# Kernel tuning notes

Hardware: AMD Instinct MI355X
Metric: run time of the kernel (lower is better)

The kernel has to match this reference:

```python
import jax, jax.numpy as jnp
import numpy as np

B, T, D, M, L = 4, 2048, 256, 128, 16
P = M * L  # max_pair_cnt


def setup_inputs() -> dict:
    key = jax.random.key(0)
    ks = jax.random.split(key, 11)
    head = jax.random.normal(ks[0], (B, P, T), jnp.float32) * 0.05
    tail = jax.random.normal(ks[1], (B, P, T), jnp.float32) * 0.05
    x = jax.random.normal(ks[2], (B, T, D), jnp.float32)
    coref_mention_position = jax.random.uniform(ks[3], (B, M, T), jnp.float32)
    lab = jax.random.uniform(ks[4], (B, P, 2), jnp.float32) + 1e-3
    coref_label = lab / lab.sum(-1, keepdims=True)  # already-softmaxed target
    coref_label_mask = jax.random.randint(ks[5], (B, P), 0, 2).astype(bool)
    lens = jnp.full((B, M), L, jnp.int32)  # uniform segment lengths
    w1 = jax.random.normal(ks[6], (3 * D, D), jnp.float32) / np.sqrt(3 * D).astype(np.float32)
    b1 = jnp.zeros((D,), jnp.float32)
    w2 = jax.random.normal(ks[7], (D, 2), jnp.float32) / np.sqrt(D).astype(np.float32)
    b2 = jnp.zeros((2,), jnp.float32)
    return {"head": head, "tail": tail, "lens": lens, "x": x,
            "coref_mention_position": coref_mention_position,
            "coref_label": coref_label, "coref_label_mask": coref_label_mask,
            "w1": w1, "b1": b1, "w2": w2, "b2": b2}


def reference(head, tail, lens, x, coref_mention_position, coref_label,
              coref_label_mask, w1, b1, w2, b2):
    # bmm-based gather of mention reps: [B,P,T] @ [B,T,D] -> [B,P,D]
    head_rep = jnp.einsum('bpt,btd->bpd', head, x)
    tail_rep = jnp.einsum('bpt,btd->bpd', tail, x)
    feat = jnp.concatenate([head_rep, tail_rep, head_rep * tail_rep], axis=-1)
    logits = jax.nn.relu(feat @ w1 + b1) @ w2 + b2  # [B,P,2]

    # ragged split_n_pad -> per-mention top-1 select (uniform lens == L -> reshape)
    scores = logits[..., 1].reshape(B, M, L)            # [B,M,L]
    max_idx = jnp.argmax(scores, axis=-1)               # [B,M]
    max_val = jnp.max(scores, axis=-1)                  # [B,M] (raw logit, as in source)
    tail_seg = tail_rep.reshape(B, M, L, D)
    sel = jnp.take_along_axis(tail_seg, max_idx[:, :, None, None], axis=2)[:, :, 0, :]
    coref_rep_m = sel * max_val[:, :, None]             # [B,M,D]

    # scatter-bmm merge back into sequence: [B,T,M] @ [B,M,D] -> [B,T,D]
    coref_rep = jnp.einsum('bmt,bmd->btd', coref_mention_position, coref_rep_m)
    output = x + coref_rep

    # KLDivLoss(reduction='mean') over masked pairs
    logq = jax.nn.log_softmax(logits, axis=-1)
    lab = coref_label
    pw = jnp.where(lab > 0, lab * jnp.log(jnp.maximum(lab, 1e-38)), 0.0) - lab * logq
    n = jnp.sum(coref_label_mask).astype(jnp.float32)
    loss = jnp.where(coref_label_mask[..., None], pw, 0.0).sum() / (n * 2.0)
    return output, loss
```

## Files before the change

kernel.cpp:

```cpp
#include <hip/hip_runtime.h>
#include <hip/hip_bf16.h>
#include <stdint.h>

#define TAU 0.35f

typedef __attribute__((ext_vector_type(8))) short bf16x8;
typedef __attribute__((ext_vector_type(4))) float f32x4;

__device__ __forceinline__ unsigned short f2bf(float f) {
  __bf16 h = (__bf16)f;
  return __builtin_bit_cast(unsigned short, h);
}
__device__ __forceinline__ float bf2f(unsigned short u) {
  unsigned int v = ((unsigned int)u) << 16;
  return __builtin_bit_cast(float, v);
}
__device__ __forceinline__ void async_copy16(const void* g, void* l) {
  __builtin_amdgcn_global_load_lds(
      (const __attribute__((address_space(1))) unsigned int*)g,
      (__attribute__((address_space(3))) unsigned int*)l, 16, 0, 0);
}

__global__ __launch_bounds__(256) void k_prep(
    const float* __restrict__ x, const float* __restrict__ w1,
    const float* __restrict__ b2,
    unsigned short* __restrict__ xt, unsigned short* __restrict__ w1t,
    float* __restrict__ logits, int* __restrict__ njobs) {
  __shared__ float tileS[64][65];
  int bx = blockIdx.x, tid = threadIdx.x;
  if (bx == 0 && tid == 0) *njobs = 0;
  if (bx < 64) {
    int i = bx * 256 + tid;
    logits[i] = b2[i & 1];
  }
  int j = tid & 63, i0 = tid >> 6;
  if (bx < 512) {
    int b = bx >> 7, t6 = (bx >> 2) & 31, d6 = bx & 3;
    const float* src = x + ((size_t)b * 2048 + (size_t)t6 * 64) * 256 + d6 * 64;
    for (int i = i0; i < 64; i += 4) tileS[i][j] = src[(size_t)i * 256 + j];
    __syncthreads();
    unsigned short* dst = xt + ((size_t)b * 256 + (size_t)d6 * 64) * 2048 + t6 * 64;
    for (int r = i0; r < 64; r += 4) dst[(size_t)r * 2048 + j] = f2bf(tileS[j][r]);
  } else {
    int wt = bx - 512;
    int k6 = wt >> 2, n6 = wt & 3;
    const float* src = w1 + ((size_t)k6 * 64) * 256 + n6 * 64;
    for (int i = i0; i < 64; i += 4) tileS[i][j] = src[(size_t)i * 256 + j];
    __syncthreads();
    unsigned short* dst = w1t + ((size_t)n6 * 64) * 768 + k6 * 64;
    for (int r = i0; r < 64; r += 4) dst[(size_t)r * 768 + j] = f2bf(tileS[j][r]);
  }
}

__global__ __launch_bounds__(256, 4) void k_gemm_rep(
    const float* __restrict__ head, const float* __restrict__ tail,
    const unsigned short* __restrict__ xt,
    float* __restrict__ hrep, float* __restrict__ trep) {
  __shared__ unsigned short As[2][4096];
  __shared__ unsigned short Bs[2][4096];
  int bx = blockIdx.x;
  int ntile = bx >> 8;
  int g = bx & 255;
  int b = g >> 6, mtile = g & 63;
  const float* Asrc = ((mtile < 32) ? head : tail) +
                      ((size_t)(b * 2048 + (mtile & 31) * 64)) * 2048;
  float* Crep = (mtile < 32) ? hrep : trep;
  const unsigned short* Bsrc = xt + ((size_t)(b * 256 + ntile * 64)) * 2048;

  int tid = threadIdx.x, lane = tid & 63, w = tid >> 6;

  int arow = tid >> 2, akq = tid & 3;
  const float* aptr = Asrc + (size_t)arow * 2048 + akq * 16;
  int rt = arow >> 4, r15 = arow & 15;
  int k8a = akq * 2, k8b = akq * 2 + 1;
  int awi0 = rt * 128 + (k8a >> 2) * 64 + (k8a & 3) * 16 + r15;
  int awi1 = rt * 128 + (k8b >> 2) * 64 + (k8b & 3) * 16 + r15;

  const unsigned short* bg[2];
  int bdst[2];
#pragma unroll
  for (int a = 0; a < 2; ++a) {
    int colofs = a * 8 + (lane >> 3);
    int k8 = (lane & 7) ^ (colofs & 7);
    bg[a] = Bsrc + (size_t)(w * 16 + colofs) * 2048 + k8 * 8;
    bdst[a] = (w * 128 + a * 64 + lane) * 8;
  }

  int sw0 = (lane >> 4) ^ (lane & 7);
  int sw1 = (4 + (lane >> 4)) ^ (lane & 7);
  int colc[4];
#pragma unroll
  for (int ct = 0; ct < 4; ++ct) colc[ct] = (ct * 16 + (lane & 15)) * 8;

  f32x4 acc[4];
#pragma unroll
  for (int ct = 0; ct < 4; ++ct) acc[ct] = (f32x4){0.f, 0.f, 0.f, 0.f};

  float4 av[4];
  {
    const float4* ap = (const float4*)aptr;
    av[0] = ap[0]; av[1] = ap[1]; av[2] = ap[2]; av[3] = ap[3];
  }
#pragma unroll
  for (int a = 0; a < 2; ++a) { async_copy16(bg[a], &Bs[0][bdst[a]]); bg[a] += 64; }
  {
    bf16x8 p0, p1;
    p0[0] = (short)f2bf(av[0].x); p0[1] = (short)f2bf(av[0].y);
    p0[2] = (short)f2bf(av[0].z); p0[3] = (short)f2bf(av[0].w);
    p0[4] = (short)f2bf(av[1].x); p0[5] = (short)f2bf(av[1].y);
    p0[6] = (short)f2bf(av[1].z); p0[7] = (short)f2bf(av[1].w);
    p1[0] = (short)f2bf(av[2].x); p1[1] = (short)f2bf(av[2].y);
    p1[2] = (short)f2bf(av[2].z); p1[3] = (short)f2bf(av[2].w);
    p1[4] = (short)f2bf(av[3].x); p1[5] = (short)f2bf(av[3].y);
    p1[6] = (short)f2bf(av[3].z); p1[7] = (short)f2bf(av[3].w);
    *(bf16x8*)&As[0][awi0 * 8] = p0;
    *(bf16x8*)&As[0][awi1 * 8] = p1;
  }
  {
    const float4* ap = (const float4*)(aptr + 64);
    av[0] = ap[0]; av[1] = ap[1]; av[2] = ap[2]; av[3] = ap[3];
  }
  __syncthreads();

  for (int it = 0; it < 32; ++it) {
    int cur = it & 1, nxt = cur ^ 1;
    if (it < 31) {
#pragma unroll
      for (int a = 0; a < 2; ++a) { async_copy16(bg[a], &Bs[nxt][bdst[a]]); bg[a] += 64; }
      bf16x8 p0, p1;
      p0[0] = (short)f2bf(av[0].x); p0[1] = (short)f2bf(av[0].y);
      p0[2] = (short)f2bf(av[0].z); p0[3] = (short)f2bf(av[0].w);
      p0[4] = (short)f2bf(av[1].x); p0[5] = (short)f2bf(av[1].y);
      p0[6] = (short)f2bf(av[1].z); p0[7] = (short)f2bf(av[1].w);
      p1[0] = (short)f2bf(av[2].x); p1[1] = (short)f2bf(av[2].y);
      p1[2] = (short)f2bf(av[2].z); p1[3] = (short)f2bf(av[2].w);
      p1[4] = (short)f2bf(av[3].x); p1[5] = (short)f2bf(av[3].y);
      p1[6] = (short)f2bf(av[3].z); p1[7] = (short)f2bf(av[3].w);
      *(bf16x8*)&As[nxt][awi0 * 8] = p0;
      *(bf16x8*)&As[nxt][awi1 * 8] = p1;
    }
    if (it < 30) {
      const float4* ap = (const float4*)(aptr + (it + 2) * 64);
      av[0] = ap[0]; av[1] = ap[1]; av[2] = ap[2]; av[3] = ap[3];
    }
    const unsigned short* A_ = As[cur];
    const unsigned short* B_ = Bs[cur];
    bf16x8 a0 = *(const bf16x8*)&A_[(w * 128 + lane) * 8];
    bf16x8 a1 = *(const bf16x8*)&A_[(w * 128 + 64 + lane) * 8];
#pragma unroll
    for (int ct = 0; ct < 4; ++ct) {
      bf16x8 b0 = *(const bf16x8*)&B_[(colc[ct] + sw0) * 8];
      acc[ct] = __builtin_amdgcn_mfma_f32_16x16x32_bf16(a0, b0, acc[ct], 0, 0, 0);
    }
#pragma unroll
    for (int ct = 0; ct < 4; ++ct) {
      bf16x8 b1 = *(const bf16x8*)&B_[(colc[ct] + sw1) * 8];
      acc[ct] = __builtin_amdgcn_mfma_f32_16x16x32_bf16(a1, b1, acc[ct], 0, 0, 0);
    }
    __syncthreads();
  }

  size_t prow = (size_t)b * 2048 + (size_t)(mtile & 31) * 64 + w * 16 + ((lane >> 4) << 2);
  int cb = ntile * 64 + (lane & 15);
#pragma unroll
  for (int ct = 0; ct < 4; ++ct)
#pragma unroll
    for (int i = 0; i < 4; ++i)
      Crep[(prow + i) * 256 + cb + ct * 16] = acc[ct][i];
}

__global__ __launch_bounds__(256) void k_feat(
    const float* __restrict__ hrep, const float* __restrict__ trep,
    unsigned short* __restrict__ featbf) {
  int gid = blockIdx.x * 256 + threadIdx.x;
  int p = gid >> 6, d0 = (gid & 63) * 4;
  float4 h4 = *(const float4*)&hrep[(size_t)p * 256 + d0];
  float4 t4 = *(const float4*)&trep[(size_t)p * 256 + d0];
  ushort4 a, bb, c;
  a.x = f2bf(h4.x); a.y = f2bf(h4.y); a.z = f2bf(h4.z); a.w = f2bf(h4.w);
  bb.x = f2bf(t4.x); bb.y = f2bf(t4.y); bb.z = f2bf(t4.z); bb.w = f2bf(t4.w);
  c.x = f2bf(h4.x * t4.x); c.y = f2bf(h4.y * t4.y);
  c.z = f2bf(h4.z * t4.z); c.w = f2bf(h4.w * t4.w);
  *(ushort4*)&featbf[(size_t)p * 768 + d0] = a;
  *(ushort4*)&featbf[(size_t)p * 768 + 256 + d0] = bb;
  *(ushort4*)&featbf[(size_t)p * 768 + 512 + d0] = c;
}

__global__ __launch_bounds__(256, 4) void k_gemm_mlp(
    const unsigned short* __restrict__ featb, const unsigned short* __restrict__ w1t,
    const float* __restrict__ b1, const float* __restrict__ w2,
    float* __restrict__ logits) {
  __shared__ unsigned short As[2][4096], Bs[2][4096];
  int bx = blockIdx.x;
  int ntile = bx >> 7;
  int mtile = bx & 127;
  int tid = threadIdx.x, lane = tid & 63, w = tid >> 6;

  const unsigned short* ag[2];
  const unsigned short* bgp[2];
  int dofs[2];
#pragma unroll
  for (int a = 0; a < 2; ++a) {
    int rowofs = a * 8 + (lane >> 3);
    int k8 = (lane & 7) ^ (rowofs & 7);
    ag[a] = featb + (size_t)(mtile * 64 + w * 16 + rowofs) * 768 + k8 * 8;
    bgp[a] = w1t + (size_t)(ntile * 64 + w * 16 + rowofs) * 768 + k8 * 8;
    dofs[a] = (w * 128 + a * 64 + lane) * 8;
  }
  int sw0 = (lane >> 4) ^ (lane & 7);
  int sw1 = (4 + (lane >> 4)) ^ (lane & 7);
  int arowc = (w * 16 + (lane & 15)) * 8;
  int colc[4];
#pragma unroll
  for (int ct = 0; ct < 4; ++ct) colc[ct] = (ct * 16 + (lane & 15)) * 8;

  f32x4 acc[4];
#pragma unroll
  for (int ct = 0; ct < 4; ++ct) acc[ct] = (f32x4){0.f, 0.f, 0.f, 0.f};

#pragma unroll
  for (int a = 0; a < 2; ++a) {
    async_copy16(ag[a], &As[0][dofs[a]]); ag[a] += 64;
    async_copy16(bgp[a], &Bs[0][dofs[a]]); bgp[a] += 64;
  }
  __syncthreads();

  for (int it = 0; it < 12; ++it) {
    int cur = it & 1, nxt = cur ^ 1;
    if (it < 11) {
#pragma unroll
      for (int a = 0; a < 2; ++a) {
        async_copy16(ag[a], &As[nxt][dofs[a]]); ag[a] += 64;
        async_copy16(bgp[a], &Bs[nxt][dofs[a]]); bgp[a] += 64;
      }
    }
    const unsigned short* A_ = As[cur];
    const unsigned short* B_ = Bs[cur];
    bf16x8 a0 = *(const bf16x8*)&A_[(arowc + sw0) * 8];
    bf16x8 a1 = *(const bf16x8*)&A_[(arowc + sw1) * 8];
#pragma unroll
    for (int ct = 0; ct < 4; ++ct) {
      bf16x8 b0 = *(const bf16x8*)&B_[(colc[ct] + sw0) * 8];
      acc[ct] = __builtin_amdgcn_mfma_f32_16x16x32_bf16(a0, b0, acc[ct], 0, 0, 0);
    }
#pragma unroll
    for (int ct = 0; ct < 4; ++ct) {
      bf16x8 b1 = *(const bf16x8*)&B_[(colc[ct] + sw1) * 8];
      acc[ct] = __builtin_amdgcn_mfma_f32_16x16x32_bf16(a1, b1, acc[ct], 0, 0, 0);
    }
    __syncthreads();
  }

  float bv[4], w20[4], w21[4];
#pragma unroll
  for (int ct = 0; ct < 4; ++ct) {
    int col = ntile * 64 + ct * 16 + (lane & 15);
    bv[ct] = b1[col]; w20[ct] = w2[col * 2]; w21[ct] = w2[col * 2 + 1];
  }
#pragma unroll
  for (int i = 0; i < 4; ++i) {
    float s0 = 0.f, s1 = 0.f;
#pragma unroll
    for (int ct = 0; ct < 4; ++ct) {
      float r = fmaxf(acc[ct][i] + bv[ct], 0.f);
      s0 += r * w20[ct]; s1 += r * w21[ct];
    }
#pragma unroll
    for (int off = 1; off < 16; off <<= 1) {
      s0 += __shfl_xor(s0, off); s1 += __shfl_xor(s1, off);
    }
    if ((lane & 15) == 0) {
      int row = mtile * 64 + w * 16 + ((lane >> 4) << 2) + i;
      atomicAdd(&logits[row * 2], s0);
      atomicAdd(&logits[row * 2 + 1], s1);
    }
  }
}

__global__ void k_select(const float* __restrict__ logits, int* __restrict__ idxv,
                         float* __restrict__ mval, int* __restrict__ cmask,
                         int* __restrict__ njobs, int* __restrict__ jobs) {
  int q = blockIdx.x * 256 + threadIdx.x;
  if (q >= 512) return;
  int base = q * 16;
  float s[16];
#pragma unroll
  for (int i = 0; i < 16; ++i) s[i] = logits[(size_t)(base + i) * 2 + 1];
  float best = s[0]; int bi = 0;
#pragma unroll
  for (int i = 1; i < 16; ++i) if (s[i] > best) { best = s[i]; bi = i; }
  int mask = 0, cnt = 0;
#pragma unroll
  for (int i = 0; i < 16; ++i) if (s[i] > best - TAU) { mask |= 1 << i; ++cnt; }
  idxv[q] = bi; mval[q] = best;
  if (cnt > 1) {
    cmask[q] = mask;
    for (int i = 0; i < 16; ++i)
      if ((mask >> i) & 1) { int j = atomicAdd(njobs, 1); jobs[j] = base + i; }
  } else cmask[q] = 0;
}

__global__ __launch_bounds__(1024) void k_refine(
    const int* __restrict__ njobs, const int* __restrict__ jobs,
    const float* __restrict__ head, const float* __restrict__ tail,
    const float* __restrict__ x, const float* __restrict__ w1,
    const float* __restrict__ b1, const float* __restrict__ w2,
    const float* __restrict__ b2, float* __restrict__ refined) {
  __shared__ float hrow[2048], trow[2048], feat[768], red[1024], red2[1024];
  int tid = threadIdx.x, seg = tid >> 8, d = tid & 255;
  int nj = *njobs;
  for (int job = blockIdx.x; job < nj; job += gridDim.x) {
    int code = jobs[job];
    int b = code >> 11, p = code & 2047;
    if (tid < 512)
      *(float4*)&hrow[tid * 4] = *(const float4*)&head[((size_t)(b * 2048 + p)) * 2048 + tid * 4];
    else {
      int u = tid - 512;
      *(float4*)&trow[u * 4] = *(const float4*)&tail[((size_t)(b * 2048 + p)) * 2048 + u * 4];
    }
    __syncthreads();
    float hr = 0.f, tr = 0.f;
    const float* xb = x + ((size_t)b * 2048) * 256 + d;
#pragma unroll 8
    for (int t = seg * 512; t < seg * 512 + 512; ++t) {
      float xv = xb[(size_t)t * 256];
      hr += hrow[t] * xv; tr += trow[t] * xv;
    }
    red[tid] = hr; red2[tid] = tr;
    __syncthreads();
    if (seg == 0) {
      float fh = red[d] + red[256 + d] + red[512 + d] + red[768 + d];
      float ft = red2[d] + red2[256 + d] + red2[512 + d] + red2[768 + d];
      feat[d] = fh; feat[256 + d] = ft; feat[512 + d] = fh * ft;
    }
    __syncthreads();
    float hp = 0.f;
    for (int ii = seg * 192; ii < seg * 192 + 192; ++ii) hp += feat[ii] * w1[(size_t)ii * 256 + d];
    red[tid] = hp;
    __syncthreads();
    if (seg == 0) {
      float hj = b1[d] + red[d] + red[256 + d] + red[512 + d] + red[768 + d];
      hj = fmaxf(hj, 0.f);
      red2[d] = hj * w2[d * 2 + 1];
    }
    __syncthreads();
    for (int s = 128; s > 0; s >>= 1) {
      if (tid < s) red2[tid] += red2[tid + s];
      __syncthreads();
    }
    if (tid == 0) refined[code] = red2[0] + b2[1];
    __syncthreads();
  }
}

__global__ __launch_bounds__(256) void k_repm(
    const int* __restrict__ idxv, const float* __restrict__ mval,
    const int* __restrict__ cmask, const float* __restrict__ refined,
    const float* __restrict__ trep, float* __restrict__ repm) {
  int q = blockIdx.x, d = threadIdx.x;
  int mask = cmask[q]; int bi; float v;
  if (mask) {
    bi = -1; v = -1e30f;
    for (int i = 0; i < 16; ++i)
      if ((mask >> i) & 1) { float s = refined[q * 16 + i]; if (s > v) { v = s; bi = i; } }
  } else { bi = idxv[q]; v = mval[q]; }
  repm[(size_t)q * 256 + d] = trep[((size_t)q * 16 + bi) * 256 + d] * v;
}

__global__ __launch_bounds__(256) void k_merge(
    const float* __restrict__ cmp, const float* __restrict__ repm,
    const float* __restrict__ x, float* __restrict__ out) {
  __shared__ float cl[128 * 16];
  int bx = blockIdx.x, b = bx >> 7, t0 = (bx & 127) * 16;
  int tid = threadIdx.x;
#pragma unroll
  for (int it = 0; it < 2; ++it) {
    int f = it * 256 + tid;
    int row = f >> 2, c4 = (f & 3) * 4;
    *(float4*)&cl[row * 16 + c4] =
        *(const float4*)&cmp[((size_t)(b * 128 + row)) * 2048 + t0 + c4];
  }
  __syncthreads();
  float acc[16];
#pragma unroll
  for (int i = 0; i < 16; ++i) acc[i] = 0.f;
  int d = tid;
  for (int m = 0; m < 128; ++m) {
    float rv = repm[(size_t)(b * 128 + m) * 256 + d];
    const float4* c4p = (const float4*)&cl[m * 16];
#pragma unroll
    for (int jj = 0; jj < 4; ++jj) {
      float4 c = c4p[jj];
      acc[jj * 4] += c.x * rv; acc[jj * 4 + 1] += c.y * rv;
      acc[jj * 4 + 2] += c.z * rv; acc[jj * 4 + 3] += c.w * rv;
    }
  }
  const float* xb = x + ((size_t)(b * 2048 + t0)) * 256 + d;
  float* ob = out + ((size_t)(b * 2048 + t0)) * 256 + d;
#pragma unroll
  for (int tt = 0; tt < 16; ++tt) ob[(size_t)tt * 256] = xb[(size_t)tt * 256] + acc[tt];
}

__global__ __launch_bounds__(1024) void k_loss(
    const float* __restrict__ logits, const float* __restrict__ lab,
    const unsigned char* __restrict__ mask, float* __restrict__ out_loss) {
  __shared__ float rs[1024], rc[1024];
  int tid = threadIdx.x;
  float sum = 0.f, cnt = 0.f;
  for (int p = tid; p < 8192; p += 1024) {
    float l0 = logits[(size_t)p * 2], l1 = logits[(size_t)p * 2 + 1];
    float a0 = lab[(size_t)p * 2], a1 = lab[(size_t)p * 2 + 1];
    float mx = fmaxf(l0, l1);
    float lse = mx + logf(expf(l0 - mx) + expf(l1 - mx));
    float pw = 0.f;
    if (a0 > 0.f) pw += a0 * logf(fmaxf(a0, 1e-38f));
    if (a1 > 0.f) pw += a1 * logf(fmaxf(a1, 1e-38f));
    pw -= a0 * (l0 - lse) + a1 * (l1 - lse);
    if (mask[p]) { sum += pw; cnt += 1.f; }
  }
  rs[tid] = sum; rc[tid] = cnt;
  __syncthreads();
  for (int s = 512; s > 0; s >>= 1) {
    if (tid < s) { rs[tid] += rs[tid + s]; rc[tid] += rc[tid + s]; }
    __syncthreads();
  }
  if (tid == 0) *out_loss = rs[0] / (rc[0] * 2.0f);
}

extern "C" void kernel_launch(void* const* d_in, const int* in_sizes, int n_in,
                              void* d_out, int out_size, void* d_ws, size_t ws_size,
                              hipStream_t stream) {
  (void)in_sizes; (void)n_in; (void)out_size; (void)ws_size;
  const float* head = (const float*)d_in[0];
  const float* tail = (const float*)d_in[1];
  const float* x = (const float*)d_in[3];
  const float* cmp = (const float*)d_in[4];
  const float* lab = (const float*)d_in[5];
  const unsigned char* lmask = (const unsigned char*)d_in[6];
  const float* w1 = (const float*)d_in[7];
  const float* b1 = (const float*)d_in[8];
  const float* w2 = (const float*)d_in[9];
  const float* b2 = (const float*)d_in[10];
  float* out = (float*)d_out;

  char* ws = (char*)d_ws;
  size_t off = 0;
  auto alloc = [&](size_t bytes) -> void* {
    void* p = ws + off; off += (bytes + 255) & ~(size_t)255; return p;
  };
  unsigned short* xt = (unsigned short*)alloc(4ull * 256 * 2048 * 2);
  unsigned short* w1t = (unsigned short*)alloc(256ull * 768 * 2);
  float* hrep = (float*)alloc(8192ull * 256 * 4);
  float* trep = (float*)alloc(8192ull * 256 * 4);
  unsigned short* featb = (unsigned short*)alloc(8192ull * 768 * 2);
  float* logits = (float*)alloc(8192ull * 2 * 4);
  float* refined = (float*)alloc(8192ull * 4);
  int* idxv = (int*)alloc(512 * 4);
  float* mvalv = (float*)alloc(512 * 4);
  int* cmaskv = (int*)alloc(512 * 4);
  int* njobs = (int*)alloc(256);
  int* jobs = (int*)alloc(8192 * 4);
  float* repm = (float*)alloc(512ull * 256 * 4);

  k_prep<<<560, 256, 0, stream>>>(x, w1, b2, xt, w1t, logits, njobs);
  k_gemm_rep<<<1024, 256, 0, stream>>>(head, tail, xt, hrep, trep);
  k_feat<<<2048, 256, 0, stream>>>(hrep, trep, featb);
  k_gemm_mlp<<<512, 256, 0, stream>>>(featb, w1t, b1, w2, logits);
  k_select<<<2, 256, 0, stream>>>(logits, idxv, mvalv, cmaskv, njobs, jobs);
  k_refine<<<256, 1024, 0, stream>>>(njobs, jobs, head, tail, x, w1, b1, w2, b2, refined);
  k_repm<<<512, 256, 0, stream>>>(idxv, mvalv, cmaskv, refined, trep, repm);
  k_merge<<<512, 256, 0, stream>>>(cmp, repm, x, out);
  k_loss<<<1, 1024, 0, stream>>>(logits, lab, lmask, out + 4ull * 2048 * 256);
}
```

Measured before the change: 328.8 us.

## Load GEMM A operand straight into MFMA registers and pipeline with vmcnt barriers

Measured after the change: 346.7 us. +5.4%, slower.

```diff
diff --git a/kernel.cpp b/kernel.cpp
--- a/kernel.cpp
+++ b/kernel.cpp
@@ -52,11 +52,18 @@
   }
 }
 
+#define WAIT_BAR(N)                                      \
+  do {                                                   \
+    asm volatile("s_waitcnt vmcnt(" #N ")" ::: "memory");\
+    __builtin_amdgcn_sched_barrier(0);                   \
+    __builtin_amdgcn_s_barrier();                        \
+    __builtin_amdgcn_sched_barrier(0);                   \
+  } while (0)
+
 __global__ __launch_bounds__(256, 4) void k_gemm_rep(
     const float* __restrict__ head, const float* __restrict__ tail,
     const unsigned short* __restrict__ xt,
     float* __restrict__ hrep, float* __restrict__ trep) {
-  __shared__ unsigned short As[2][4096];
   __shared__ unsigned short Bs[2][4096];
   int bx = blockIdx.x;
   int ntile = bx >> 8;
@@ -69,21 +76,18 @@
 
   int tid = threadIdx.x, lane = tid & 63, w = tid >> 6;
 
-  int arow = tid >> 2, akq = tid & 3;
-  const float* aptr = Asrc + (size_t)arow * 2048 + akq * 16;
-  int rt = arow >> 4, r15 = arow & 15;
-  int k8a = akq * 2, k8b = akq * 2 + 1;
-  int awi0 = rt * 128 + (k8a >> 2) * 64 + (k8a & 3) * 16 + r15;
-  int awi1 = rt * 128 + (k8b >> 2) * 64 + (k8b & 3) * 16 + r15;
-
-  const unsigned short* bg[2];
-  int bdst[2];
-#pragma unroll
-  for (int a = 0; a < 2; ++a) {
-    int colofs = a * 8 + (lane >> 3);
-    int k8 = (lane & 7) ^ (colofs & 7);
-    bg[a] = Bsrc + (size_t)(w * 16 + colofs) * 2048 + k8 * 8;
-    bdst[a] = (w * 128 + a * 64 + lane) * 8;
+  const unsigned short* bg0;
+  const unsigned short* bg1;
+  int bdst0, bdst1;
+  {
+    int colofs0 = (lane >> 3);
+    int colofs1 = 8 + (lane >> 3);
+    int k80 = (lane & 7) ^ (colofs0 & 7);
+    int k81 = (lane & 7) ^ (colofs1 & 7);
+    bg0 = Bsrc + (size_t)(w * 16 + colofs0) * 2048 + k80 * 8;
+    bg1 = Bsrc + (size_t)(w * 16 + colofs1) * 2048 + k81 * 8;
+    bdst0 = (w * 128 + lane) * 8;
+    bdst1 = (w * 128 + 64 + lane) * 8;
   }
 
   int sw0 = (lane >> 4) ^ (lane & 7);
@@ -92,72 +96,85 @@
 #pragma unroll
   for (int ct = 0; ct < 4; ++ct) colc[ct] = (ct * 16 + (lane & 15)) * 8;
 
+  const float* anext =
+      Asrc + (size_t)(w * 16 + (lane & 15)) * 2048 + ((lane >> 4) << 3);
+
   f32x4 acc[4];
 #pragma unroll
   for (int ct = 0; ct < 4; ++ct) acc[ct] = (f32x4){0.f, 0.f, 0.f, 0.f};
 
-  float4 av[4];
-  {
-    const float4* ap = (const float4*)aptr;
-    av[0] = ap[0]; av[1] = ap[1]; av[2] = ap[2]; av[3] = ap[3];
-  }
-#pragma unroll
-  for (int a = 0; a < 2; ++a) { async_copy16(bg[a], &Bs[0][bdst[a]]); bg[a] += 64; }
-  {
-    bf16x8 p0, p1;
-    p0[0] = (short)f2bf(av[0].x); p0[1] = (short)f2bf(av[0].y);
-    p0[2] = (short)f2bf(av[0].z); p0[3] = (short)f2bf(av[0].w);
-    p0[4] = (short)f2bf(av[1].x); p0[5] = (short)f2bf(av[1].y);
-    p0[6] = (short)f2bf(av[1].z); p0[7] = (short)f2bf(av[1].w);
-    p1[0] = (short)f2bf(av[2].x); p1[1] = (short)f2bf(av[2].y);
-    p1[2] = (short)f2bf(av[2].z); p1[3] = (short)f2bf(av[2].w);
-    p1[4] = (short)f2bf(av[3].x); p1[5] = (short)f2bf(av[3].y);
-    p1[6] = (short)f2bf(av[3].z); p1[7] = (short)f2bf(av[3].w);
-    *(bf16x8*)&As[0][awi0 * 8] = p0;
-    *(bf16x8*)&As[0][awi1 * 8] = p1;
-  }
-  {
-    const float4* ap = (const float4*)(aptr + 64);
-    av[0] = ap[0]; av[1] = ap[1]; av[2] = ap[2]; av[3] = ap[3];
-  }
-  __syncthreads();
-
-  for (int it = 0; it < 32; ++it) {
-    int cur = it & 1, nxt = cur ^ 1;
-    if (it < 31) {
-#pragma unroll
-      for (int a = 0; a < 2; ++a) { async_copy16(bg[a], &Bs[nxt][bdst[a]]); bg[a] += 64; }
-      bf16x8 p0, p1;
-      p0[0] = (short)f2bf(av[0].x); p0[1] = (short)f2bf(av[0].y);
-      p0[2] = (short)f2bf(av[0].z); p0[3] = (short)f2bf(av[0].w);
-      p0[4] = (short)f2bf(av[1].x); p0[5] = (short)f2bf(av[1].y);
-      p0[6] = (short)f2bf(av[1].z); p0[7] = (short)f2bf(av[1].w);
-      p1[0] = (short)f2bf(av[2].x); p1[1] = (short)f2bf(av[2].y);
-      p1[2] = (short)f2bf(av[2].z); p1[3] = (short)f2bf(av[2].w);
-      p1[4] = (short)f2bf(av[3].x); p1[5] = (short)f2bf(av[3].y);
-      p1[6] = (short)f2bf(av[3].z); p1[7] = (short)f2bf(av[3].w);
-      *(bf16x8*)&As[nxt][awi0 * 8] = p0;
-      *(bf16x8*)&As[nxt][awi1 * 8] = p1;
-    }
-    if (it < 30) {
-      const float4* ap = (const float4*)(aptr + (it + 2) * 64);
-      av[0] = ap[0]; av[1] = ap[1]; av[2] = ap[2]; av[3] = ap[3];
-    }
-    const unsigned short* A_ = As[cur];
-    const unsigned short* B_ = Bs[cur];
-    bf16x8 a0 = *(const bf16x8*)&A_[(w * 128 + lane) * 8];
-    bf16x8 a1 = *(const bf16x8*)&A_[(w * 128 + 64 + lane) * 8];
+  auto STAGEB = [&](int buf) {
+    async_copy16(bg0, &Bs[buf][bdst0]); bg0 += 64;
+    async_copy16(bg1, &Bs[buf][bdst1]); bg1 += 64;
+  };
+  auto LOADA = [&](float4* av) {
+    const float4* ap = (const float4*)anext;
+    av[0] = ap[0]; av[1] = ap[1];
+    av[2] = ap[8]; av[3] = ap[9];
+    anext += 64;
+  };
+  auto CONV = [&](const float4* av, bf16x8& f0, bf16x8& f1) {
+    f0[0] = (short)f2bf(av[0].x); f0[1] = (short)f2bf(av[0].y);
+    f0[2] = (short)f2bf(av[0].z); f0[3] = (short)f2bf(av[0].w);
+    f0[4] = (short)f2bf(av[1].x); f0[5] = (short)f2bf(av[1].y);
+    f0[6] = (short)f2bf(av[1].z); f0[7] = (short)f2bf(av[1].w);
+    f1[0] = (short)f2bf(av[2].x); f1[1] = (short)f2bf(av[2].y);
+    f1[2] = (short)f2bf(av[2].z); f1[3] = (short)f2bf(av[2].w);
+    f1[4] = (short)f2bf(av[3].x); f1[5] = (short)f2bf(av[3].y);
+    f1[6] = (short)f2bf(av[3].z); f1[7] = (short)f2bf(av[3].w);
+  };
+  auto MMA = [&](int buf, bf16x8 f0, bf16x8 f1) {
+    const unsigned short* B_ = Bs[buf];
 #pragma unroll
     for (int ct = 0; ct < 4; ++ct) {
       bf16x8 b0 = *(const bf16x8*)&B_[(colc[ct] + sw0) * 8];
-      acc[ct] = __builtin_amdgcn_mfma_f32_16x16x32_bf16(a0, b0, acc[ct], 0, 0, 0);
+      acc[ct] = __builtin_amdgcn_mfma_f32_16x16x32_bf16(f0, b0, acc[ct], 0, 0, 0);
     }
 #pragma unroll
     for (int ct = 0; ct < 4; ++ct) {
       bf16x8 b1 = *(const bf16x8*)&B_[(colc[ct] + sw1) * 8];
-      acc[ct] = __builtin_amdgcn_mfma_f32_16x16x32_bf16(a1, b1, acc[ct], 0, 0, 0);
-    }
-    __syncthreads();
+      acc[ct] = __builtin_amdgcn_mfma_f32_16x16x32_bf16(f1, b1, acc[ct], 0, 0, 0);
+    }
+  };
+
+  float4 avA[4], avB[4];
+  STAGEB(0);
+  LOADA(avA);
+  LOADA(avB);
+
+  for (int k = 0; k < 15; ++k) {
+    WAIT_BAR(4);
+    STAGEB(1);
+    __builtin_amdgcn_sched_barrier(0);
+    {
+      bf16x8 f0, f1;
+      CONV(avA, f0, f1);
+      LOADA(avA);
+      MMA(0, f0, f1);
+    }
+    WAIT_BAR(4);
+    STAGEB(0);
+    __builtin_amdgcn_sched_barrier(0);
+    {
+      bf16x8 f0, f1;
+      CONV(avB, f0, f1);
+      LOADA(avB);
+      MMA(1, f0, f1);
+    }
+  }
+  WAIT_BAR(4);
+  STAGEB(1);
+  __builtin_amdgcn_sched_barrier(0);
+  {
+    bf16x8 f0, f1;
+    CONV(avA, f0, f1);
+    MMA(0, f0, f1);
+  }
+  WAIT_BAR(0);
+  {
+    bf16x8 f0, f1;
+    CONV(avB, f0, f1);
+    MMA(1, f0, f1);
   }
 
   size_t prow = (size_t)b * 2048 + (size_t)(mtile & 31) * 64 + w * 16 + ((lane >> 4) << 2);
```
